# Optimization experiments

Measured on AMD Instinct MI355X. Metric: run time of the kernel, lower is better.

Reference implementation:

```python
import jax, jax.numpy as jnp
import numpy as np

HEAD_DIM = 128

def setup_inputs() -> dict:
    key = jax.random.key(0)
    k1, k2, k3 = jax.random.split(key, 3)
    B, Q, KV, H, D = 1, 2048, 2048, 32, HEAD_DIM
    q = jax.random.normal(k1, (B, Q, H, D), dtype=jnp.float32)
    k = jax.random.normal(k2, (B, KV, H, D), dtype=jnp.float32)
    v = jax.random.normal(k3, (B, KV, H, D), dtype=jnp.float32)
    # corm_mask row i is 1/(i+1), broadcast over kv_len (matches prepare())
    corm_mask = jnp.broadcast_to(1.0 / (jnp.arange(Q, dtype=jnp.float32) + 1.0)[:, None], (Q, KV))
    return {"q": q, "k": k, "v": v, "corm_mask": corm_mask}

def reference(q, k, v, corm_mask):
    B, Q, H, D = q.shape
    KV = k.shape[1]
    scale = 1.0 / jnp.sqrt(jnp.float32(D))
    # [B,H,Q,KV] attention scores
    scores = jnp.einsum('bqhd,bkhd->bhqk', q, k) * scale
    # causal mask: position i (query) attends to keys j <= i + (KV - Q)
    qi = jnp.arange(Q)[:, None]
    kj = jnp.arange(KV)[None, :]
    causal = kj <= qi + (KV - Q)  # [Q,KV]
    scores = jnp.where(causal[None, None], scores, -jnp.inf)
    probs = jax.nn.softmax(scores.astype(jnp.float32), axis=-1)
    out = jnp.einsum('bhqk,bkhd->bqhd', probs.astype(q.dtype), v)
    # per-key eviction mask: any query whose normalized prob >= threshold
    corm_score = jnp.any(probs >= corm_mask[None, None], axis=2)  # [B,H,KV]
    return out.reshape(B, Q, H, D), corm_score.reshape(B, H, KV)
```

## Files before the change

### kernel.cpp

```cpp
#include <hip/hip_runtime.h>
#include <math.h>


#define HN   32
#define DH   128
#define SEQ  2048
#define NBLK 32
#define KB   64
#define TILE_SHORTS 8192
#define SC2   0.1275174072417346f

typedef __attribute__((ext_vector_type(4))) float f4;
typedef __attribute__((ext_vector_type(8))) short s8;

__device__ __forceinline__ short f2bf(float x) {
  union { float f; unsigned u; } a; a.f = x;
  unsigned r = a.u + 0x7FFFu + ((a.u >> 16) & 1u);
  return (short)(r >> 16);
}
__device__ __forceinline__ float bf2f(short h) {
  union { unsigned u; float f; } a;
  a.u = ((unsigned)(unsigned short)h) << 16;
  return a.f;
}
__device__ __forceinline__ int swz(int row, int colShort, int Cshort) {
  int byte = (colShort * 2) ^ ((row & 7) << 4);
  return row * Cshort + (byte >> 1);
}
__device__ __forceinline__ float lanef(float v, int srcLane) {
  return __builtin_bit_cast(float,
      __builtin_amdgcn_ds_bpermute(srcLane * 4, __builtin_bit_cast(int, v)));
}

__global__ __launch_bounds__(256) void prep_qkv(
    const float* __restrict__ gQ, const float* __restrict__ gK,
    const float* __restrict__ gV, short* __restrict__ oQh,
    short* __restrict__ oQl, short* __restrict__ oKs, short* __restrict__ oVt)
{
  __shared__ short Vs[64][136];
  const int blk = blockIdx.x, h = blockIdx.y, tid = threadIdx.x;
  const size_t toff = ((size_t)h * NBLK + blk) * TILE_SHORTS;

#pragma unroll
  for (int i = 0; i < 4; ++i) {
    int f = tid + 256 * i;
    int n = f >> 8, dt = (f >> 6) & 3, l4 = (f >> 4) & 3, l15 = f & 15;
    int r = n * 16 + l15, c0 = dt * 32 + l4 * 8;
    size_t rowoff = ((size_t)(blk * 64 + r) * HN + h) * DH + c0;
    {
      f4 a = *(const f4*)(gQ + rowoff), b = *(const f4*)(gQ + rowoff + 4);
      s8 oh, ol;
#pragma unroll
      for (int e = 0; e < 4; ++e) {
        float sa = a[e] * SC2, sb = b[e] * SC2;
        short hi = f2bf(sa); oh[e] = hi; ol[e] = f2bf(sa - bf2f(hi));
        short h2 = f2bf(sb); oh[4+e] = h2; ol[4+e] = f2bf(sb - bf2f(h2));
      }
      *(s8*)&oQh[toff + (size_t)f * 8] = oh;
      *(s8*)&oQl[toff + (size_t)f * 8] = ol;
    }
    {
      f4 a = *(const f4*)(gK + rowoff), b = *(const f4*)(gK + rowoff + 4);
      s8 o;
#pragma unroll
      for (int e = 0; e < 4; ++e) { o[e] = f2bf(a[e]); o[4+e] = f2bf(b[e]); }
      *(s8*)&oKs[toff + (size_t)f * 8] = o;
    }
    {
      f4 a = *(const f4*)(gV + rowoff), b = *(const f4*)(gV + rowoff + 4);
      s8 o;
#pragma unroll
      for (int e = 0; e < 4; ++e) { o[e] = f2bf(a[e]); o[4+e] = f2bf(b[e]); }
      *(s8*)&Vs[r][c0] = o;
    }
  }
  __syncthreads();
#pragma unroll
  for (int i = 0; i < 4; ++i) {
    int f = tid + 256 * i;
    int ds = f >> 7, hf = (f >> 6) & 1, l4 = (f >> 4) & 3, l15 = f & 15;
    int d = ds * 16 + l15, k0 = hf * 32 + l4 * 8;
    s8 o;
#pragma unroll
    for (int j = 0; j < 8; ++j) o[j] = Vs[k0 + j][d];
    *(s8*)&oVt[toff + (size_t)f * 8] = o;
  }
}

__global__ __launch_bounds__(128, 2) void flash_fwd(
    const short* __restrict__ gQh, const short* __restrict__ gKs,
    const short* __restrict__ gVt, float* __restrict__ gO,
    float* __restrict__ gT)
{
  __shared__ short Ps[2][2][1024];

  const int id = blockIdx.x;
  const int xcd = id & 7, jj = id >> 3;
  const int h = xcd + 8 * (jj >> 5);
  const int b = 31 - (jj & 31);
  const int tid = threadIdx.x;
  const int wv = tid >> 6, ln = tid & 63, l15 = ln & 15, l4 = ln >> 4;
  const int q0 = b * 64 + wv * 32;
  const size_t hbase = (size_t)h * NBLK * TILE_SHORTS;
  const int ntile = b + 1;

  const short* qtile = gQh + hbase + (size_t)b * TILE_SHORTS;
  s8 qf[2][4];
#pragma unroll
  for (int g = 0; g < 2; ++g)
#pragma unroll
    for (int dt = 0; dt < 4; ++dt)
      qf[g][dt] = *(const s8*)&qtile[(size_t)((((wv * 2 + g) * 4 + dt) * 64 + ln)) * 8];

  f4 oacc[2][8];
#pragma unroll
  for (int g = 0; g < 2; ++g)
#pragma unroll
    for (int i = 0; i < 8; ++i) { oacc[g][i][0]=0.f; oacc[g][i][1]=0.f; oacc[g][i][2]=0.f; oacc[g][i][3]=0.f; }
  float m1[2] = {-INFINITY, -INFINITY}, l1[2] = {0.f, 0.f};
  const int abase = (ln & 48) + 4 * l4;

  const short* kp = gKs + hbase;
  const short* vp = gVt + hbase;

  for (int t = 0; t < ntile; ++t) {
    s8 kf[4][4];
#pragma unroll
    for (int n = 0; n < 4; ++n)
#pragma unroll
      for (int dt = 0; dt < 4; ++dt)
        kf[n][dt] = *(const s8*)&kp[(size_t)(((n * 4 + dt) * 64 + ln)) * 8];

    f4 sacc[2][4];
#pragma unroll
    for (int g = 0; g < 2; ++g)
#pragma unroll
      for (int n = 0; n < 4; ++n) { sacc[g][n][0]=0.f; sacc[g][n][1]=0.f; sacc[g][n][2]=0.f; sacc[g][n][3]=0.f; }
    __builtin_amdgcn_s_setprio(1);
#pragma unroll
    for (int n = 0; n < 4; ++n)
#pragma unroll
      for (int dt = 0; dt < 4; ++dt) {
        sacc[0][n] = __builtin_amdgcn_mfma_f32_16x16x32_bf16(kf[n][dt], qf[0][dt], sacc[0][n], 0, 0, 0);
        sacc[1][n] = __builtin_amdgcn_mfma_f32_16x16x32_bf16(kf[n][dt], qf[1][dt], sacc[1][n], 0, 0, 0);
      }
    __builtin_amdgcn_s_setprio(0);

    s8 vb[8][2];
#pragma unroll
    for (int ds = 0; ds < 8; ++ds)
#pragma unroll
      for (int hf = 0; hf < 2; ++hf)
        vb[ds][hf] = *(const s8*)&vp[(size_t)(((ds * 2 + hf) * 64 + ln)) * 8];

    if (t == b) {
#pragma unroll
      for (int g = 0; g < 2; ++g) {
        const int qg = q0 + g * 16 + l15;
#pragma unroll
        for (int n = 0; n < 4; ++n)
#pragma unroll
          for (int j = 0; j < 4; ++j) {
            int kv = t * 64 + n * 16 + 4 * l4 + j;
            if (kv > qg) sacc[g][n][j] = -INFINITY;
          }
      }
    }
    float mt[2], alpha[2], mold[2];
#pragma unroll
    for (int g = 0; g < 2; ++g) {
      float a0 = fmaxf(fmaxf(sacc[g][0][0], sacc[g][0][1]), fmaxf(sacc[g][0][2], sacc[g][0][3]));
      float a1 = fmaxf(fmaxf(sacc[g][1][0], sacc[g][1][1]), fmaxf(sacc[g][1][2], sacc[g][1][3]));
      float a2 = fmaxf(fmaxf(sacc[g][2][0], sacc[g][2][1]), fmaxf(sacc[g][2][2], sacc[g][2][3]));
      float a3 = fmaxf(fmaxf(sacc[g][3][0], sacc[g][3][1]), fmaxf(sacc[g][3][2], sacc[g][3][3]));
      float m = fmaxf(fmaxf(a0, a1), fmaxf(a2, a3));
      m = fmaxf(m, __shfl_xor(m, 16));
      m = fmaxf(m, __shfl_xor(m, 32));
      mt[g] = m;
      mold[g] = m1[g];
      float mn = fmaxf(m1[g], m);
      alpha[g] = __builtin_amdgcn_exp2f(m1[g] - mn);
      m1[g] = mn;
      float s0 = 0.f;
#pragma unroll
      for (int n = 0; n < 4; ++n) {
#pragma unroll
        for (int j = 0; j < 4; ++j) sacc[g][n][j] = __builtin_amdgcn_exp2f(sacc[g][n][j] - mn);
        s0 += (sacc[g][n][0] + sacc[g][n][1]) + (sacc[g][n][2] + sacc[g][n][3]);
      }
      s0 += __shfl_xor(s0, 16);
      s0 += __shfl_xor(s0, 32);
      l1[g] = l1[g] * alpha[g] + s0;
    }

    if (__any((mt[0] > mold[0]) || (mt[1] > mold[1]))) {
#pragma unroll
      for (int g = 0; g < 2; ++g) {
        float aj[4];
#pragma unroll
        for (int j = 0; j < 4; ++j) aj[j] = lanef(alpha[g], abase + j);
#pragma unroll
        for (int ds = 0; ds < 8; ++ds)
#pragma unroll
          for (int j = 0; j < 4; ++j) oacc[g][ds][j] *= aj[j];
      }
    }

#pragma unroll
    for (int g = 0; g < 2; ++g) {
      short* pw = &Ps[wv][g][0];
#pragma unroll
      for (int n = 0; n < 4; ++n) {
        unsigned lo, hi;
        asm("v_cvt_pk_bf16_f32 %0, %1, %2" : "=v"(lo) : "v"(sacc[g][n][0]), "v"(sacc[g][n][1]));
        asm("v_cvt_pk_bf16_f32 %0, %1, %2" : "=v"(hi) : "v"(sacc[g][n][2]), "v"(sacc[g][n][3]));
        uint2 w; w.x = lo; w.y = hi;
        *(uint2*)&pw[swz(l15, n * 16 + 4 * l4, KB)] = w;
      }
    }

    s8 pa00 = *(const s8*)&Ps[wv][0][swz(l15, l4 * 8, KB)];
    s8 pa01 = *(const s8*)&Ps[wv][0][swz(l15, 32 + l4 * 8, KB)];
    s8 pa10 = *(const s8*)&Ps[wv][1][swz(l15, l4 * 8, KB)];
    s8 pa11 = *(const s8*)&Ps[wv][1][swz(l15, 32 + l4 * 8, KB)];
    __builtin_amdgcn_s_setprio(1);
#pragma unroll
    for (int ds = 0; ds < 8; ++ds) {
      oacc[0][ds] = __builtin_amdgcn_mfma_f32_16x16x32_bf16(pa00, vb[ds][0], oacc[0][ds], 0, 0, 0);
      oacc[1][ds] = __builtin_amdgcn_mfma_f32_16x16x32_bf16(pa10, vb[ds][0], oacc[1][ds], 0, 0, 0);
      oacc[0][ds] = __builtin_amdgcn_mfma_f32_16x16x32_bf16(pa01, vb[ds][1], oacc[0][ds], 0, 0, 0);
      oacc[1][ds] = __builtin_amdgcn_mfma_f32_16x16x32_bf16(pa11, vb[ds][1], oacc[1][ds], 0, 0, 0);
    }
    __builtin_amdgcn_s_setprio(0);
    kp += TILE_SHORTS; vp += TILE_SHORTS;
  }

#pragma unroll
  for (int g = 0; g < 2; ++g) {
    float linv = 1.0f / l1[g];
    float lj[4];
#pragma unroll
    for (int j = 0; j < 4; ++j) lj[j] = lanef(linv, abase + j);
#pragma unroll
    for (int j = 0; j < 4; ++j) {
      int qg = q0 + g * 16 + 4 * l4 + j;
      float* orow = gO + ((size_t)qg * HN + h) * DH;
#pragma unroll
      for (int ds = 0; ds < 8; ++ds)
        orow[ds * 16 + l15] = oacc[g][ds][j] * lj[j];
    }
    if (l4 == 0) {
      int qg = q0 + g * 16 + l15;
      gT[h * SEQ + qg] = m1[g] + log2f(l1[g]) - log2f((float)(qg + 1));
    }
  }
}

__global__ __launch_bounds__(128, 2) void corm_fwd(
    const float* __restrict__ gK, const short* __restrict__ gQh,
    const short* __restrict__ gQl, const float* __restrict__ gT,
    float* __restrict__ gC)
{
  __shared__ float Tt[SEQ];

  const int id = blockIdx.x;
  const int xcd = id & 7, jj = id >> 3;
  const int h = xcd + 8 * (jj >> 5);
  const int kvb = (jj & 31) * 64;
  const int tid = threadIdx.x;
  const int wv = tid >> 6, ln = tid & 63, l15 = ln & 15, l4 = ln >> 4;
  const int kvw = kvb + wv * 32;
  const int t0 = kvb >> 6;

  for (int i = tid; i < (NBLK - t0) * 64; i += 128)
    Tt[i] = gT[h * SEQ + t0 * 64 + i];

  s8 khi[2][4], klo[2][4];
#pragma unroll
  for (int g = 0; g < 2; ++g) {
    const float* krow = gK + ((size_t)(kvw + g * 16 + l15) * HN + h) * DH;
#pragma unroll
    for (int dt = 0; dt < 4; ++dt) {
      f4 a = *(const f4*)(krow + dt * 32 + l4 * 8);
      f4 bb = *(const f4*)(krow + dt * 32 + l4 * 8 + 4);
#pragma unroll
      for (int e = 0; e < 4; ++e) {
        short hi = f2bf(a[e]); khi[g][dt][e] = hi; klo[g][dt][e] = f2bf(a[e] - bf2f(hi));
        short h2 = f2bf(bb[e]); khi[g][dt][4+e] = h2; klo[g][dt][4+e] = f2bf(bb[e] - bf2f(h2));
      }
    }
  }
  __syncthreads();

  const size_t hbase = (size_t)h * NBLK * TILE_SHORTS;
  int fired[2][4] = {{0,0,0,0},{0,0,0,0}};

  for (int t = t0; t < NBLK; ++t) {
    const short* qht = gQh + hbase + (size_t)t * TILE_SHORTS;
    const short* qlt = gQl + hbase + (size_t)t * TILE_SHORTS;
#pragma unroll
    for (int n = 0; n < 4; ++n) {
      s8 qhb[4], qlb[4];
#pragma unroll
      for (int dt = 0; dt < 4; ++dt) {
        qhb[dt] = *(const s8*)&qht[(size_t)(((n * 4 + dt) * 64 + ln)) * 8];
        qlb[dt] = *(const s8*)&qlt[(size_t)(((n * 4 + dt) * 64 + ln)) * 8];
      }
      f4 acc0, acc1;
      acc0[0]=0.f; acc0[1]=0.f; acc0[2]=0.f; acc0[3]=0.f;
      acc1[0]=0.f; acc1[1]=0.f; acc1[2]=0.f; acc1[3]=0.f;
      __builtin_amdgcn_s_setprio(1);
#pragma unroll
      for (int dt = 0; dt < 4; ++dt) {
        acc0 = __builtin_amdgcn_mfma_f32_16x16x32_bf16(khi[0][dt], qhb[dt], acc0, 0, 0, 0);
        acc0 = __builtin_amdgcn_mfma_f32_16x16x32_bf16(khi[0][dt], qlb[dt], acc0, 0, 0, 0);
        acc0 = __builtin_amdgcn_mfma_f32_16x16x32_bf16(klo[0][dt], qhb[dt], acc0, 0, 0, 0);
        acc1 = __builtin_amdgcn_mfma_f32_16x16x32_bf16(khi[1][dt], qhb[dt], acc1, 0, 0, 0);
        acc1 = __builtin_amdgcn_mfma_f32_16x16x32_bf16(khi[1][dt], qlb[dt], acc1, 0, 0, 0);
        acc1 = __builtin_amdgcn_mfma_f32_16x16x32_bf16(klo[1][dt], qhb[dt], acc1, 0, 0, 0);
      }
      __builtin_amdgcn_s_setprio(0);
      int qg = t * 64 + n * 16 + l15;
      float Tq = Tt[qg - t0 * 64];
#pragma unroll
      for (int j = 0; j < 4; ++j) {
        int kvr0 = kvw + 4 * l4 + j;
        if (qg >= kvr0 && acc0[j] >= Tq) fired[0][j] = 1;
        int kvr1 = kvw + 16 + 4 * l4 + j;
        if (qg >= kvr1 && acc1[j] >= Tq) fired[1][j] = 1;
      }
    }
  }

#pragma unroll
  for (int g = 0; g < 2; ++g)
#pragma unroll
    for (int j = 0; j < 4; ++j) {
      fired[g][j] |= __shfl_xor(fired[g][j], 1, 16);
      fired[g][j] |= __shfl_xor(fired[g][j], 2, 16);
      fired[g][j] |= __shfl_xor(fired[g][j], 4, 16);
      fired[g][j] |= __shfl_xor(fired[g][j], 8, 16);
    }
  if (l15 == 0) {
#pragma unroll
    for (int g = 0; g < 2; ++g)
#pragma unroll
      for (int j = 0; j < 4; ++j)
        gC[h * SEQ + kvw + g * 16 + 4 * l4 + j] = fired[g][j] ? 1.0f : 0.0f;
  }
}

extern "C" void kernel_launch(void* const* d_in, const int* in_sizes, int n_in,
                              void* d_out, int out_size, void* d_ws, size_t ws_size,
                              hipStream_t stream) {
  const float* q = (const float*)d_in[0];
  const float* k = (const float*)d_in[1];
  const float* v = (const float*)d_in[2];
  float* out  = (float*)d_out;
  float* corm = out + (size_t)SEQ * HN * DH;

  const size_t ARR = (size_t)HN * NBLK * TILE_SHORTS;
  short* Qh = (short*)d_ws;
  short* Ql = Qh + ARR;
  short* Ks = Ql + ARR;
  short* Vt = Ks + ARR;
  float* T  = (float*)(Vt + ARR);

  prep_qkv<<<dim3(NBLK, HN), dim3(256), 0, stream>>>(q, k, v, Qh, Ql, Ks, Vt);
  flash_fwd<<<dim3(1024), dim3(128), 0, stream>>>(Qh, Ks, Vt, out, T);
  corm_fwd<<<dim3(1024), dim3(128), 0, stream>>>(k, Qh, Ql, T, corm);
}
```

Before: 182.1 us.

## Software-pipeline Q loads in corm kernel and hoist V loads in attention loop

In the attention loop, the V fragment loads now start before the QK MFMAs, so their latency overlaps with the matrix work. In the corm kernel, the nested tile and sub-tile loop becomes a flat loop with double-buffered Q hi/lo fragment loads, so the next fragment's loads are issued before the current MFMAs. The three split-precision products now go into six independent accumulators instead of two dependent chains, which raises MFMA-level parallelism. The cost is higher register pressure, the extra adds at the end, and a slightly different floating-point summation order in the threshold comparison.

```diff
diff --git a/kernel.cpp b/kernel.cpp
--- a/kernel.cpp
+++ b/kernel.cpp
@@ -130,6 +130,12 @@
 #pragma unroll
       for (int dt = 0; dt < 4; ++dt)
         kf[n][dt] = *(const s8*)&kp[(size_t)(((n * 4 + dt) * 64 + ln)) * 8];
+    s8 vb[8][2];
+#pragma unroll
+    for (int ds = 0; ds < 8; ++ds)
+#pragma unroll
+      for (int hf = 0; hf < 2; ++hf)
+        vb[ds][hf] = *(const s8*)&vp[(size_t)(((ds * 2 + hf) * 64 + ln)) * 8];
 
     f4 sacc[2][4];
 #pragma unroll
@@ -145,13 +151,6 @@
         sacc[1][n] = __builtin_amdgcn_mfma_f32_16x16x32_bf16(kf[n][dt], qf[1][dt], sacc[1][n], 0, 0, 0);
       }
     __builtin_amdgcn_s_setprio(0);
-
-    s8 vb[8][2];
-#pragma unroll
-    for (int ds = 0; ds < 8; ++ds)
-#pragma unroll
-      for (int hf = 0; hf < 2; ++hf)
-        vb[ds][hf] = *(const s8*)&vp[(size_t)(((ds * 2 + hf) * 64 + ln)) * 8];
 
     if (t == b) {
 #pragma unroll
@@ -271,9 +270,10 @@
   const int wv = tid >> 6, ln = tid & 63, l15 = ln & 15, l4 = ln >> 4;
   const int kvw = kvb + wv * 32;
   const int t0 = kvb >> 6;
-
-  for (int i = tid; i < (NBLK - t0) * 64; i += 128)
-    Tt[i] = gT[h * SEQ + t0 * 64 + i];
+  const int total = (NBLK - t0) * 4;
+
+  for (int i = tid; i < total * 16; i += 128)
+    Tt[i] = gT[h * SEQ + kvb + i];
 
   s8 khi[2][4], klo[2][4];
 #pragma unroll
@@ -293,44 +293,60 @@
   __syncthreads();
 
   const size_t hbase = (size_t)h * NBLK * TILE_SHORTS;
+  const short* qhflat = gQh + hbase + (size_t)t0 * TILE_SHORTS;
+  const short* qlflat = gQl + hbase + (size_t)t0 * TILE_SHORTS;
+  const int lnoff = ln * 8;
+
   int fired[2][4] = {{0,0,0,0},{0,0,0,0}};
 
-  for (int t = t0; t < NBLK; ++t) {
-    const short* qht = gQh + hbase + (size_t)t * TILE_SHORTS;
-    const short* qlt = gQl + hbase + (size_t)t * TILE_SHORTS;
-#pragma unroll
-    for (int n = 0; n < 4; ++n) {
-      s8 qhb[4], qlb[4];
-#pragma unroll
-      for (int dt = 0; dt < 4; ++dt) {
-        qhb[dt] = *(const s8*)&qht[(size_t)(((n * 4 + dt) * 64 + ln)) * 8];
-        qlb[dt] = *(const s8*)&qlt[(size_t)(((n * 4 + dt) * 64 + ln)) * 8];
-      }
-      f4 acc0, acc1;
-      acc0[0]=0.f; acc0[1]=0.f; acc0[2]=0.f; acc0[3]=0.f;
-      acc1[0]=0.f; acc1[1]=0.f; acc1[2]=0.f; acc1[3]=0.f;
-      __builtin_amdgcn_s_setprio(1);
-#pragma unroll
-      for (int dt = 0; dt < 4; ++dt) {
-        acc0 = __builtin_amdgcn_mfma_f32_16x16x32_bf16(khi[0][dt], qhb[dt], acc0, 0, 0, 0);
-        acc0 = __builtin_amdgcn_mfma_f32_16x16x32_bf16(khi[0][dt], qlb[dt], acc0, 0, 0, 0);
-        acc0 = __builtin_amdgcn_mfma_f32_16x16x32_bf16(klo[0][dt], qhb[dt], acc0, 0, 0, 0);
-        acc1 = __builtin_amdgcn_mfma_f32_16x16x32_bf16(khi[1][dt], qhb[dt], acc1, 0, 0, 0);
-        acc1 = __builtin_amdgcn_mfma_f32_16x16x32_bf16(khi[1][dt], qlb[dt], acc1, 0, 0, 0);
-        acc1 = __builtin_amdgcn_mfma_f32_16x16x32_bf16(klo[1][dt], qhb[dt], acc1, 0, 0, 0);
-      }
-      __builtin_amdgcn_s_setprio(0);
-      int qg = t * 64 + n * 16 + l15;
-      float Tq = Tt[qg - t0 * 64];
-#pragma unroll
-      for (int j = 0; j < 4; ++j) {
-        int kvr0 = kvw + 4 * l4 + j;
-        if (qg >= kvr0 && acc0[j] >= Tq) fired[0][j] = 1;
-        int kvr1 = kvw + 16 + 4 * l4 + j;
-        if (qg >= kvr1 && acc1[j] >= Tq) fired[1][j] = 1;
-      }
-    }
-  }
+#define CORM_LOAD(QH_, QL_, idx_) do {                                        \
+    size_t o_ = (size_t)(idx_) * 2048 + lnoff;                                \
+    _Pragma("unroll")                                                         \
+    for (int dt = 0; dt < 4; ++dt) {                                          \
+      QH_[dt] = *(const s8*)&qhflat[o_ + dt * 512];                           \
+      QL_[dt] = *(const s8*)&qlflat[o_ + dt * 512];                           \
+    }                                                                         \
+  } while (0)
+
+#define CORM_STEP(QH_, QL_, idx_) do {                                       \
+    float Tq_ = Tt[(idx_) * 16 + l15];                                       \
+    f4 hh0, hl0, lh0, hh1, hl1, lh1;                                         \
+    hh0[0]=0.f; hh0[1]=0.f; hh0[2]=0.f; hh0[3]=0.f;                          \
+    hl0 = hh0; lh0 = hh0; hh1 = hh0; hl1 = hh0; lh1 = hh0;                   \
+    __builtin_amdgcn_s_setprio(1);                                           \
+    _Pragma("unroll")                                                        \
+    for (int dt = 0; dt < 4; ++dt) {                                         \
+      hh0 = __builtin_amdgcn_mfma_f32_16x16x32_bf16(khi[0][dt], QH_[dt], hh0, 0, 0, 0); \
+      hh1 = __builtin_amdgcn_mfma_f32_16x16x32_bf16(khi[1][dt], QH_[dt], hh1, 0, 0, 0); \
+      hl0 = __builtin_amdgcn_mfma_f32_16x16x32_bf16(khi[0][dt], QL_[dt], hl0, 0, 0, 0); \
+      hl1 = __builtin_amdgcn_mfma_f32_16x16x32_bf16(khi[1][dt], QL_[dt], hl1, 0, 0, 0); \
+      lh0 = __builtin_amdgcn_mfma_f32_16x16x32_bf16(klo[0][dt], QH_[dt], lh0, 0, 0, 0); \
+      lh1 = __builtin_amdgcn_mfma_f32_16x16x32_bf16(klo[1][dt], QH_[dt], lh1, 0, 0, 0); \
+    }                                                                        \
+    __builtin_amdgcn_s_setprio(0);                                           \
+    f4 acc0_ = (hh0 + hl0) + lh0;                                            \
+    f4 acc1_ = (hh1 + hl1) + lh1;                                            \
+    int qg_ = kvb + (idx_) * 16 + l15;                                       \
+    _Pragma("unroll")                                                        \
+    for (int j = 0; j < 4; ++j) {                                            \
+      int kvr0_ = kvw + 4 * l4 + j;                                          \
+      if (qg_ >= kvr0_ && acc0_[j] >= Tq_) fired[0][j] = 1;                  \
+      int kvr1_ = kvw + 16 + 4 * l4 + j;                                     \
+      if (qg_ >= kvr1_ && acc1_[j] >= Tq_) fired[1][j] = 1;                  \
+    }                                                                        \
+  } while (0)
+
+  s8 qA[4], lA[4], qB[4], lB[4];
+  CORM_LOAD(qA, lA, 0);
+  for (int i = 0; i < total; i += 2) {
+    CORM_LOAD(qB, lB, i + 1);
+    CORM_STEP(qA, lA, i);
+    int i2 = (i + 2 < total) ? i + 2 : i;
+    CORM_LOAD(qA, lA, i2);
+    CORM_STEP(qB, lB, i + 1);
+  }
+#undef CORM_LOAD
+#undef CORM_STEP
 
 #pragma unroll
   for (int g = 0; g < 2; ++g)
```

New measurement: 187.1 us. +2.8%, slower.

## Halve flash query rows per wave and split corm scan into chunks

Applied to the files above, without the earlier changes.

The flash kernel now gives each wave 16 query rows instead of 32 and launches twice as many blocks, so the causal workload is spread more evenly. The corm kernel is split along the query-tile axis into chunks of at most four tiles per block. The corm output is zeroed in the prep kernel and only fired entries are written, which lets blocks covering different chunks of the same keys combine their results. Each K/V tile is now loaded for half as many query rows, so global and cache traffic per unit of work goes up, and the corm kernel reloads K once per chunk.

```diff
diff --git a/kernel.cpp b/kernel.cpp
--- a/kernel.cpp
+++ b/kernel.cpp
@@ -35,11 +35,14 @@
 __global__ __launch_bounds__(256) void prep_qkv(
     const float* __restrict__ gQ, const float* __restrict__ gK,
     const float* __restrict__ gV, short* __restrict__ oQh,
-    short* __restrict__ oQl, short* __restrict__ oKs, short* __restrict__ oVt)
+    short* __restrict__ oQl, short* __restrict__ oKs, short* __restrict__ oVt,
+    float* __restrict__ oC)
 {
   __shared__ short Vs[64][136];
   const int blk = blockIdx.x, h = blockIdx.y, tid = threadIdx.x;
   const size_t toff = ((size_t)h * NBLK + blk) * TILE_SHORTS;
+
+  if (tid < 64) oC[h * SEQ + blk * 64 + tid] = 0.f;
 
 #pragma unroll
   for (int i = 0; i < 4; ++i) {
@@ -87,37 +90,34 @@
   }
 }
 
-__global__ __launch_bounds__(128, 2) void flash_fwd(
+__global__ __launch_bounds__(128) void flash_fwd(
     const short* __restrict__ gQh, const short* __restrict__ gKs,
     const short* __restrict__ gVt, float* __restrict__ gO,
     float* __restrict__ gT)
 {
-  __shared__ short Ps[2][2][1024];
+  __shared__ short Ps[2][1024];
 
   const int id = blockIdx.x;
   const int xcd = id & 7, jj = id >> 3;
-  const int h = xcd + 8 * (jj >> 5);
-  const int b = 31 - (jj & 31);
+  const int h = xcd + 8 * (jj >> 6);
+  const int b32 = 63 - (jj & 63);
   const int tid = threadIdx.x;
   const int wv = tid >> 6, ln = tid & 63, l15 = ln & 15, l4 = ln >> 4;
-  const int q0 = b * 64 + wv * 32;
+  const int q0 = b32 * 32 + wv * 16;
   const size_t hbase = (size_t)h * NBLK * TILE_SHORTS;
-  const int ntile = b + 1;
-
-  const short* qtile = gQh + hbase + (size_t)b * TILE_SHORTS;
-  s8 qf[2][4];
-#pragma unroll
-  for (int g = 0; g < 2; ++g)
-#pragma unroll
-    for (int dt = 0; dt < 4; ++dt)
-      qf[g][dt] = *(const s8*)&qtile[(size_t)((((wv * 2 + g) * 4 + dt) * 64 + ln)) * 8];
-
-  f4 oacc[2][8];
-#pragma unroll
-  for (int g = 0; g < 2; ++g)
-#pragma unroll
-    for (int i = 0; i < 8; ++i) { oacc[g][i][0]=0.f; oacc[g][i][1]=0.f; oacc[g][i][2]=0.f; oacc[g][i][3]=0.f; }
-  float m1[2] = {-INFINITY, -INFINITY}, l1[2] = {0.f, 0.f};
+  const int ntile = (q0 >> 6) + 1;
+
+  const short* qtile = gQh + hbase + (size_t)(q0 >> 6) * TILE_SHORTS;
+  const int nq = (q0 >> 4) & 3;
+  s8 qf[4];
+#pragma unroll
+  for (int dt = 0; dt < 4; ++dt)
+    qf[dt] = *(const s8*)&qtile[(size_t)(((nq * 4 + dt) * 64 + ln)) * 8];
+
+  f4 oacc[8];
+#pragma unroll
+  for (int i = 0; i < 8; ++i) { oacc[i][0]=0.f; oacc[i][1]=0.f; oacc[i][2]=0.f; oacc[i][3]=0.f; }
+  float m1 = -INFINITY, l1 = 0.f;
   const int abase = (ln & 48) + 4 * l4;
 
   const short* kp = gKs + hbase;
@@ -130,22 +130,6 @@
 #pragma unroll
       for (int dt = 0; dt < 4; ++dt)
         kf[n][dt] = *(const s8*)&kp[(size_t)(((n * 4 + dt) * 64 + ln)) * 8];
-
-    f4 sacc[2][4];
-#pragma unroll
-    for (int g = 0; g < 2; ++g)
-#pragma unroll
-      for (int n = 0; n < 4; ++n) { sacc[g][n][0]=0.f; sacc[g][n][1]=0.f; sacc[g][n][2]=0.f; sacc[g][n][3]=0.f; }
-    __builtin_amdgcn_s_setprio(1);
-#pragma unroll
-    for (int n = 0; n < 4; ++n)
-#pragma unroll
-      for (int dt = 0; dt < 4; ++dt) {
-        sacc[0][n] = __builtin_amdgcn_mfma_f32_16x16x32_bf16(kf[n][dt], qf[0][dt], sacc[0][n], 0, 0, 0);
-        sacc[1][n] = __builtin_amdgcn_mfma_f32_16x16x32_bf16(kf[n][dt], qf[1][dt], sacc[1][n], 0, 0, 0);
-      }
-    __builtin_amdgcn_s_setprio(0);
-
     s8 vb[8][2];
 #pragma unroll
     for (int ds = 0; ds < 8; ++ds)
@@ -153,127 +137,119 @@
       for (int hf = 0; hf < 2; ++hf)
         vb[ds][hf] = *(const s8*)&vp[(size_t)(((ds * 2 + hf) * 64 + ln)) * 8];
 
-    if (t == b) {
-#pragma unroll
-      for (int g = 0; g < 2; ++g) {
-        const int qg = q0 + g * 16 + l15;
-#pragma unroll
-        for (int n = 0; n < 4; ++n)
-#pragma unroll
-          for (int j = 0; j < 4; ++j) {
-            int kv = t * 64 + n * 16 + 4 * l4 + j;
-            if (kv > qg) sacc[g][n][j] = -INFINITY;
-          }
-      }
-    }
-    float mt[2], alpha[2], mold[2];
-#pragma unroll
-    for (int g = 0; g < 2; ++g) {
-      float a0 = fmaxf(fmaxf(sacc[g][0][0], sacc[g][0][1]), fmaxf(sacc[g][0][2], sacc[g][0][3]));
-      float a1 = fmaxf(fmaxf(sacc[g][1][0], sacc[g][1][1]), fmaxf(sacc[g][1][2], sacc[g][1][3]));
-      float a2 = fmaxf(fmaxf(sacc[g][2][0], sacc[g][2][1]), fmaxf(sacc[g][2][2], sacc[g][2][3]));
-      float a3 = fmaxf(fmaxf(sacc[g][3][0], sacc[g][3][1]), fmaxf(sacc[g][3][2], sacc[g][3][3]));
-      float m = fmaxf(fmaxf(a0, a1), fmaxf(a2, a3));
-      m = fmaxf(m, __shfl_xor(m, 16));
-      m = fmaxf(m, __shfl_xor(m, 32));
-      mt[g] = m;
-      mold[g] = m1[g];
-      float mn = fmaxf(m1[g], m);
-      alpha[g] = __builtin_amdgcn_exp2f(m1[g] - mn);
-      m1[g] = mn;
-      float s0 = 0.f;
-#pragma unroll
-      for (int n = 0; n < 4; ++n) {
-#pragma unroll
-        for (int j = 0; j < 4; ++j) sacc[g][n][j] = __builtin_amdgcn_exp2f(sacc[g][n][j] - mn);
-        s0 += (sacc[g][n][0] + sacc[g][n][1]) + (sacc[g][n][2] + sacc[g][n][3]);
-      }
-      s0 += __shfl_xor(s0, 16);
-      s0 += __shfl_xor(s0, 32);
-      l1[g] = l1[g] * alpha[g] + s0;
-    }
-
-    if (__any((mt[0] > mold[0]) || (mt[1] > mold[1]))) {
-#pragma unroll
-      for (int g = 0; g < 2; ++g) {
-        float aj[4];
-#pragma unroll
-        for (int j = 0; j < 4; ++j) aj[j] = lanef(alpha[g], abase + j);
-#pragma unroll
-        for (int ds = 0; ds < 8; ++ds)
-#pragma unroll
-          for (int j = 0; j < 4; ++j) oacc[g][ds][j] *= aj[j];
-      }
-    }
-
-#pragma unroll
-    for (int g = 0; g < 2; ++g) {
-      short* pw = &Ps[wv][g][0];
-#pragma unroll
-      for (int n = 0; n < 4; ++n) {
-        unsigned lo, hi;
-        asm("v_cvt_pk_bf16_f32 %0, %1, %2" : "=v"(lo) : "v"(sacc[g][n][0]), "v"(sacc[g][n][1]));
-        asm("v_cvt_pk_bf16_f32 %0, %1, %2" : "=v"(hi) : "v"(sacc[g][n][2]), "v"(sacc[g][n][3]));
-        uint2 w; w.x = lo; w.y = hi;
-        *(uint2*)&pw[swz(l15, n * 16 + 4 * l4, KB)] = w;
-      }
-    }
-
-    s8 pa00 = *(const s8*)&Ps[wv][0][swz(l15, l4 * 8, KB)];
-    s8 pa01 = *(const s8*)&Ps[wv][0][swz(l15, 32 + l4 * 8, KB)];
-    s8 pa10 = *(const s8*)&Ps[wv][1][swz(l15, l4 * 8, KB)];
-    s8 pa11 = *(const s8*)&Ps[wv][1][swz(l15, 32 + l4 * 8, KB)];
+    f4 sacc[4];
+#pragma unroll
+    for (int n = 0; n < 4; ++n) { sacc[n][0]=0.f; sacc[n][1]=0.f; sacc[n][2]=0.f; sacc[n][3]=0.f; }
     __builtin_amdgcn_s_setprio(1);
 #pragma unroll
+    for (int n = 0; n < 4; ++n)
+#pragma unroll
+      for (int dt = 0; dt < 4; ++dt)
+        sacc[n] = __builtin_amdgcn_mfma_f32_16x16x32_bf16(kf[n][dt], qf[dt], sacc[n], 0, 0, 0);
+    __builtin_amdgcn_s_setprio(0);
+
+    if (t == ntile - 1) {
+      const int qg = q0 + l15;
+#pragma unroll
+      for (int n = 0; n < 4; ++n)
+#pragma unroll
+        for (int j = 0; j < 4; ++j) {
+          int kv = t * 64 + n * 16 + 4 * l4 + j;
+          if (kv > qg) sacc[n][j] = -INFINITY;
+        }
+    }
+
+    float a0 = fmaxf(fmaxf(sacc[0][0], sacc[0][1]), fmaxf(sacc[0][2], sacc[0][3]));
+    float a1 = fmaxf(fmaxf(sacc[1][0], sacc[1][1]), fmaxf(sacc[1][2], sacc[1][3]));
+    float a2 = fmaxf(fmaxf(sacc[2][0], sacc[2][1]), fmaxf(sacc[2][2], sacc[2][3]));
+    float a3 = fmaxf(fmaxf(sacc[3][0], sacc[3][1]), fmaxf(sacc[3][2], sacc[3][3]));
+    float mt = fmaxf(fmaxf(a0, a1), fmaxf(a2, a3));
+    mt = fmaxf(mt, __shfl_xor(mt, 16));
+    mt = fmaxf(mt, __shfl_xor(mt, 32));
+    float mold = m1;
+    float mn = fmaxf(m1, mt);
+    float alpha = __builtin_amdgcn_exp2f(m1 - mn);
+    m1 = mn;
+    float s0 = 0.f;
+#pragma unroll
+    for (int n = 0; n < 4; ++n) {
+#pragma unroll
+      for (int j = 0; j < 4; ++j) sacc[n][j] = __builtin_amdgcn_exp2f(sacc[n][j] - mn);
+      s0 += (sacc[n][0] + sacc[n][1]) + (sacc[n][2] + sacc[n][3]);
+    }
+    s0 += __shfl_xor(s0, 16);
+    s0 += __shfl_xor(s0, 32);
+    l1 = l1 * alpha + s0;
+
+    if (__any(mt > mold)) {
+      float aj[4];
+#pragma unroll
+      for (int j = 0; j < 4; ++j) aj[j] = lanef(alpha, abase + j);
+#pragma unroll
+      for (int ds = 0; ds < 8; ++ds)
+#pragma unroll
+        for (int j = 0; j < 4; ++j) oacc[ds][j] *= aj[j];
+    }
+
+    short* pw = Ps[wv];
+#pragma unroll
+    for (int n = 0; n < 4; ++n) {
+      unsigned lo, hi;
+      asm("v_cvt_pk_bf16_f32 %0, %1, %2" : "=v"(lo) : "v"(sacc[n][0]), "v"(sacc[n][1]));
+      asm("v_cvt_pk_bf16_f32 %0, %1, %2" : "=v"(hi) : "v"(sacc[n][2]), "v"(sacc[n][3]));
+      uint2 w; w.x = lo; w.y = hi;
+      *(uint2*)&pw[swz(l15, n * 16 + 4 * l4, KB)] = w;
+    }
+
+    s8 pa0 = *(const s8*)&pw[swz(l15, l4 * 8, KB)];
+    s8 pa1 = *(const s8*)&pw[swz(l15, 32 + l4 * 8, KB)];
+    __builtin_amdgcn_s_setprio(1);
+#pragma unroll
     for (int ds = 0; ds < 8; ++ds) {
-      oacc[0][ds] = __builtin_amdgcn_mfma_f32_16x16x32_bf16(pa00, vb[ds][0], oacc[0][ds], 0, 0, 0);
-      oacc[1][ds] = __builtin_amdgcn_mfma_f32_16x16x32_bf16(pa10, vb[ds][0], oacc[1][ds], 0, 0, 0);
-      oacc[0][ds] = __builtin_amdgcn_mfma_f32_16x16x32_bf16(pa01, vb[ds][1], oacc[0][ds], 0, 0, 0);
-      oacc[1][ds] = __builtin_amdgcn_mfma_f32_16x16x32_bf16(pa11, vb[ds][1], oacc[1][ds], 0, 0, 0);
+      oacc[ds] = __builtin_amdgcn_mfma_f32_16x16x32_bf16(pa0, vb[ds][0], oacc[ds], 0, 0, 0);
+      oacc[ds] = __builtin_amdgcn_mfma_f32_16x16x32_bf16(pa1, vb[ds][1], oacc[ds], 0, 0, 0);
     }
     __builtin_amdgcn_s_setprio(0);
     kp += TILE_SHORTS; vp += TILE_SHORTS;
   }
 
-#pragma unroll
-  for (int g = 0; g < 2; ++g) {
-    float linv = 1.0f / l1[g];
-    float lj[4];
-#pragma unroll
-    for (int j = 0; j < 4; ++j) lj[j] = lanef(linv, abase + j);
-#pragma unroll
-    for (int j = 0; j < 4; ++j) {
-      int qg = q0 + g * 16 + 4 * l4 + j;
-      float* orow = gO + ((size_t)qg * HN + h) * DH;
-#pragma unroll
-      for (int ds = 0; ds < 8; ++ds)
-        orow[ds * 16 + l15] = oacc[g][ds][j] * lj[j];
-    }
-    if (l4 == 0) {
-      int qg = q0 + g * 16 + l15;
-      gT[h * SEQ + qg] = m1[g] + log2f(l1[g]) - log2f((float)(qg + 1));
-    }
-  }
-}
-
-__global__ __launch_bounds__(128, 2) void corm_fwd(
+  float linv = 1.0f / l1;
+  float lj[4];
+#pragma unroll
+  for (int j = 0; j < 4; ++j) lj[j] = lanef(linv, abase + j);
+#pragma unroll
+  for (int j = 0; j < 4; ++j) {
+    int qg = q0 + 4 * l4 + j;
+    float* orow = gO + ((size_t)qg * HN + h) * DH;
+#pragma unroll
+    for (int ds = 0; ds < 8; ++ds)
+      orow[ds * 16 + l15] = oacc[ds][j] * lj[j];
+  }
+  if (l4 == 0) {
+    int qg = q0 + l15;
+    gT[h * SEQ + qg] = m1 + log2f(l1) - log2f((float)(qg + 1));
+  }
+}
+
+__global__ __launch_bounds__(128) void corm_fwd(
     const float* __restrict__ gK, const short* __restrict__ gQh,
     const short* __restrict__ gQl, const float* __restrict__ gT,
     float* __restrict__ gC)
 {
-  __shared__ float Tt[SEQ];
-
-  const int id = blockIdx.x;
-  const int xcd = id & 7, jj = id >> 3;
-  const int h = xcd + 8 * (jj >> 5);
-  const int kvb = (jj & 31) * 64;
+  __shared__ float Tt[256];
+
+  const int h = blockIdx.x, m = blockIdx.y, c = blockIdx.z;
+  const int tb = m + 4 * c;
+  if (tb >= NBLK) return;
+  const int te = (tb + 4 < NBLK) ? tb + 4 : NBLK;
+  const int kvb = m * 64;
+
   const int tid = threadIdx.x;
   const int wv = tid >> 6, ln = tid & 63, l15 = ln & 15, l4 = ln >> 4;
   const int kvw = kvb + wv * 32;
-  const int t0 = kvb >> 6;
-
-  for (int i = tid; i < (NBLK - t0) * 64; i += 128)
-    Tt[i] = gT[h * SEQ + t0 * 64 + i];
+
+  for (int i = tid; i < (te - tb) * 64; i += 128)
+    Tt[i] = gT[h * SEQ + tb * 64 + i];
 
   s8 khi[2][4], klo[2][4];
 #pragma unroll
@@ -295,9 +271,14 @@
   const size_t hbase = (size_t)h * NBLK * TILE_SHORTS;
   int fired[2][4] = {{0,0,0,0},{0,0,0,0}};
 
-  for (int t = t0; t < NBLK; ++t) {
+  for (int t = tb; t < te; ++t) {
     const short* qht = gQh + hbase + (size_t)t * TILE_SHORTS;
     const short* qlt = gQl + hbase + (size_t)t * TILE_SHORTS;
+    float Tq4[4];
+#pragma unroll
+    for (int n = 0; n < 4; ++n)
+      Tq4[n] = Tt[(t - tb) * 64 + n * 16 + l15];
+
 #pragma unroll
     for (int n = 0; n < 4; ++n) {
       s8 qhb[4], qlb[4];
@@ -308,7 +289,7 @@
       }
       f4 acc0, acc1;
       acc0[0]=0.f; acc0[1]=0.f; acc0[2]=0.f; acc0[3]=0.f;
-      acc1[0]=0.f; acc1[1]=0.f; acc1[2]=0.f; acc1[3]=0.f;
+      acc1 = acc0;
       __builtin_amdgcn_s_setprio(1);
 #pragma unroll
       for (int dt = 0; dt < 4; ++dt) {
@@ -321,7 +302,7 @@
       }
       __builtin_amdgcn_s_setprio(0);
       int qg = t * 64 + n * 16 + l15;
-      float Tq = Tt[qg - t0 * 64];
+      float Tq = Tq4[n];
 #pragma unroll
       for (int j = 0; j < 4; ++j) {
         int kvr0 = kvw + 4 * l4 + j;
@@ -346,7 +327,8 @@
     for (int g = 0; g < 2; ++g)
 #pragma unroll
       for (int j = 0; j < 4; ++j)
-        gC[h * SEQ + kvw + g * 16 + 4 * l4 + j] = fired[g][j] ? 1.0f : 0.0f;
+        if (fired[g][j])
+          gC[h * SEQ + kvw + g * 16 + 4 * l4 + j] = 1.0f;
   }
 }
 
@@ -366,7 +348,7 @@
   short* Vt = Ks + ARR;
   float* T  = (float*)(Vt + ARR);
 
-  prep_qkv<<<dim3(NBLK, HN), dim3(256), 0, stream>>>(q, k, v, Qh, Ql, Ks, Vt);
-  flash_fwd<<<dim3(1024), dim3(128), 0, stream>>>(Qh, Ks, Vt, out, T);
-  corm_fwd<<<dim3(1024), dim3(128), 0, stream>>>(k, Qh, Ql, T, corm);
-}
+  prep_qkv<<<dim3(NBLK, HN), dim3(256), 0, stream>>>(q, k, v, Qh, Ql, Ks, Vt, corm);
+  flash_fwd<<<dim3(2048), dim3(128), 0, stream>>>(Qh, Ks, Vt, out, T);
+  corm_fwd<<<dim3(32, 32, 8), dim3(128), 0, stream>>>(k, Qh, Ql, T, corm);
+}
```

Result: faster. 177.7 us (-2.4%).
